# Performance work log

Measured on AMD Instinct MI355X. Metric: run time of the kernel, lower is better.

Reference implementation:

```python
import jax, jax.numpy as jnp
import numpy as np
import math

GROUPS = 32
EPS = 1e-5
NUM_HEADS = 8


def group_norm(x, gamma, beta):
    # x: [B, C, T]
    B, C, T = x.shape
    xg = x.reshape(B, GROUPS, C // GROUPS, T)
    mean = xg.mean(axis=(2, 3), keepdims=True)
    var = xg.var(axis=(2, 3), keepdims=True)
    xn = (xg - mean) * jax.lax.rsqrt(var + EPS)
    return xn.reshape(B, C, T) * gamma[None, :, None] + beta[None, :, None]


def qkv_attention(qkv, num_heads):
    # qkv: [B, 3C, T]
    B, C3, T = qkv.shape
    split = C3 // (3 * num_heads)  # head dim
    q, k, v = jnp.split(qkv, 3, axis=1)
    scale = 1.0 / math.sqrt(math.sqrt(split))
    q = (q * scale).reshape(B * num_heads, split, T)
    k = (k * scale).reshape(B * num_heads, split, T)
    v = v.reshape(B * num_heads, split, T)
    w = jnp.einsum('bct,bcs->bts', q, k)
    w = jax.nn.softmax(w.astype(jnp.float32), axis=-1).astype(w.dtype)
    out = jnp.einsum('bts,bcs->bct', w, v)
    return out.reshape(B, -1, T)


def setup_inputs() -> dict:
    key = jax.random.key(0)
    ks = jax.random.split(key, 6)
    B, C, H, W = 16, 512, 32, 32
    x = jax.random.normal(ks[0], (B, C, H, W), dtype=jnp.float32)
    gamma = jnp.ones((C,), jnp.float32)
    beta = jnp.zeros((C,), jnp.float32)
    w_qkv = jax.random.normal(ks[1], (3 * C, C), jnp.float32) * (1.0 / math.sqrt(C))
    b_qkv = jax.random.normal(ks[2], (3 * C,), jnp.float32) * 0.01
    # proj is zero-initialized in the module; use small random weights so the
    # full op chain (proj + residual) is numerically exercised.
    w_proj = jax.random.normal(ks[3], (C, C), jnp.float32) * (1.0 / math.sqrt(C))
    b_proj = jax.random.normal(ks[4], (C,), jnp.float32) * 0.01
    return {"x": x, "gamma": gamma, "beta": beta, "w_qkv": w_qkv,
            "b_qkv": b_qkv, "w_proj": w_proj, "b_proj": b_proj}


def reference(x, gamma, beta, w_qkv, b_qkv, w_proj, b_proj):
    b, c = x.shape[0], x.shape[1]
    spatial = x.shape[2:]
    xf = x.reshape(b, c, -1)                     # [B, C, T]
    xn = group_norm(xf, gamma, beta)
    qkv = jnp.einsum('oc,bct->bot', w_qkv, xn) + b_qkv[None, :, None]
    h = qkv_attention(qkv, NUM_HEADS)
    h = jnp.einsum('oc,bct->bot', w_proj, h) + b_proj[None, :, None]
    # NOTE: residual uses the normalized x (x is reassigned before norm in torch code)
    return (xn + h).reshape(b, c, *spatial)
```

## Files before the change

kernel.cpp:

```cpp
#include <hip/hip_runtime.h>

typedef __attribute__((ext_vector_type(8))) short s16x8;
typedef __attribute__((ext_vector_type(8))) unsigned short u16x8;
typedef __attribute__((ext_vector_type(4))) float f32x4;
typedef __attribute__((ext_vector_type(16))) float f32x16;

#define DEV static __device__ __forceinline__

DEV unsigned short f2bf(float f){
  union { float f; unsigned u; } v; v.f = f;
  unsigned u = v.u;
  return (unsigned short)((u + 0x7FFFu + ((u >> 16) & 1u)) >> 16);
}

DEV unsigned cvt_pk(float lo, float hi){
  unsigned r;
  asm("v_cvt_pk_bf16_f32 %0, %1, %2" : "=v"(r) : "v"(lo), "v"(hi));
  return r;
}

DEV void gload16(const void* g, void* l){
  __builtin_amdgcn_global_load_lds((const __attribute__((address_space(1))) void*)g,
                                   (__attribute__((address_space(3))) void*)l, 16, 0, 0);
}

DEV unsigned usel(bool c, unsigned a, unsigned b){ return c ? a : b; }

__global__ __launch_bounds__(256) void k_cvt(const float* __restrict__ src,
                                             unsigned short* __restrict__ dst, int n4){
  int i = blockIdx.x * 256 + threadIdx.x;
  if (i >= n4) return;
  float4 v = ((const float4*)src)[i];
  unsigned long long p = (unsigned long long)f2bf(v.x)
                       | ((unsigned long long)f2bf(v.y) << 16)
                       | ((unsigned long long)f2bf(v.z) << 32)
                       | ((unsigned long long)f2bf(v.w) << 48);
  *(unsigned long long*)(dst + (size_t)i * 4) = p;
}

__global__ __launch_bounds__(256) void k_gn(const float* __restrict__ x,
    const float* __restrict__ gamma, const float* __restrict__ beta,
    float* __restrict__ stats, unsigned short* __restrict__ xt){
  __shared__ unsigned short lt[1024 * 16];
  __shared__ float red[8];
  __shared__ float sh_ms[2];
  const int b = blockIdx.x >> 5, g = blockIdx.x & 31;
  const int tid = threadIdx.x;
  const float* base = x + ((size_t)(b * 512 + g * 16)) * 1024;

  float s = 0.f, ss = 0.f;
  #pragma unroll
  for (int i = 0; i < 16; ++i){
    float4 v = *(const float4*)(base + i * 1024 + tid * 4);
    s  += v.x + v.y + v.z + v.w;
    ss += v.x * v.x + v.y * v.y + v.z * v.z + v.w * v.w;
  }
  #pragma unroll
  for (int d = 1; d < 64; d <<= 1){ s += __shfl_xor(s, d); ss += __shfl_xor(ss, d); }
  if ((tid & 63) == 0){ red[tid >> 6] = s; red[4 + (tid >> 6)] = ss; }
  __syncthreads();
  if (tid == 0){
    float ts  = red[0] + red[1] + red[2] + red[3];
    float tss = red[4] + red[5] + red[6] + red[7];
    float mean = ts * (1.f / 16384.f);
    float var  = tss * (1.f / 16384.f) - mean * mean;
    float rstd = rsqrtf(var + 1e-5f);
    sh_ms[0] = mean; sh_ms[1] = rstd;
    stats[(size_t)blockIdx.x * 2] = mean;
    stats[(size_t)blockIdx.x * 2 + 1] = rstd;
  }
  __syncthreads();
  const float mean = sh_ms[0], rstd = sh_ms[1];

  unsigned short vals[4][16];
  #pragma unroll
  for (int i = 0; i < 16; ++i){
    float4 v = *(const float4*)(base + i * 1024 + tid * 4);
    float gsc = gamma[g * 16 + i] * rstd;
    float bof = beta[g * 16 + i] - mean * gsc;
    vals[0][i] = f2bf(v.x * gsc + bof);
    vals[1][i] = f2bf(v.y * gsc + bof);
    vals[2][i] = f2bf(v.z * gsc + bof);
    vals[3][i] = f2bf(v.w * gsc + bof);
  }
  #pragma unroll
  for (int k2 = 0; k2 < 4; ++k2){
    u16x8 lo, hi;
    #pragma unroll
    for (int e = 0; e < 8; ++e){ lo[e] = vals[k2][e]; hi[e] = vals[k2][8 + e]; }
    int t = tid * 4 + k2;
    *(u16x8*)&lt[t * 16]     = lo;
    *(u16x8*)&lt[t * 16 + 8] = hi;
  }
  __syncthreads();
  unsigned short* dst = xt + ((size_t)b * 1024) * 512 + g * 16;
  #pragma unroll
  for (int j = 0; j < 8; ++j){
    int idx = j * 256 + tid;
    int t = idx >> 1, half = idx & 1;
    u16x8 v = *(const u16x8*)&lt[t * 16 + half * 8];
    *(u16x8*)(dst + (size_t)t * 512 + half * 8) = v;
  }
}

DEV void gemm_mainloop(const unsigned short* __restrict__ pA,
                       const unsigned short* __restrict__ pB,
                       unsigned short* As, unsigned short* Bs,
                       f32x4 (&acc)[4][4], int tid){
  const int lane = tid & 63, wv = tid >> 6;
  const int wr = wv >> 1, wc = wv & 1;
  const int ro = lane & 15;
  for (int k0 = 0; k0 < 512; k0 += 64){
    #pragma unroll
    for (int it = 0; it < 4; ++it){
      int chunk = it * 256 + tid;
      int r = chunk >> 3, sb = chunk & 7;
      size_t goff = (size_t)r * 512 + k0 + ((sb ^ (r & 7)) << 3);
      gload16(pA + goff, As + (size_t)(it * 256 + wv * 64) * 8);
      gload16(pB + goff, Bs + (size_t)(it * 256 + wv * 64) * 8);
    }
    __syncthreads();
    #pragma unroll
    for (int kk = 0; kk < 2; ++kk){
      s16x8 a[4], bb[4];
      int ko = kk * 64 + ((lane >> 4) << 4);
      #pragma unroll
      for (int i2 = 0; i2 < 4; ++i2){
        int ra = wr * 64 + i2 * 16 + ro;
        a[i2]  = *(const s16x8*)((const char*)As + ra * 128 + (ko ^ ((ra & 7) << 4)));
        int rb = wc * 64 + i2 * 16 + ro;
        bb[i2] = *(const s16x8*)((const char*)Bs + rb * 128 + (ko ^ ((rb & 7) << 4)));
      }
      __builtin_amdgcn_s_setprio(1);
      #pragma unroll
      for (int i2 = 0; i2 < 4; ++i2)
        #pragma unroll
        for (int j2 = 0; j2 < 4; ++j2)
          acc[i2][j2] = __builtin_amdgcn_mfma_f32_16x16x32_bf16(a[i2], bb[j2], acc[i2][j2], 0, 0, 0);
      __builtin_amdgcn_s_setprio(0);
    }
    __syncthreads();
  }
}

__global__ __launch_bounds__(256) void k_qkv(const unsigned short* __restrict__ W,
    const unsigned short* __restrict__ Xt, const float* __restrict__ bias,
    unsigned short* __restrict__ qkt, unsigned short* __restrict__ vbuf){
  __shared__ unsigned short As[128 * 64], Bs[128 * 64];
  const int bid = blockIdx.x;
  const int nt = bid & 7; const int tmp = bid >> 3;
  const int mt = tmp % 12, b = tmp / 12;
  const int tid = threadIdx.x;
  const unsigned short* Wt = W + (size_t)mt * 128 * 512;
  const unsigned short* Xb = Xt + ((size_t)(b * 1024) + nt * 128) * 512;
  f32x4 acc[4][4];
  #pragma unroll
  for (int i = 0; i < 4; ++i)
    #pragma unroll
    for (int j = 0; j < 4; ++j) acc[i][j] = f32x4{0.f, 0.f, 0.f, 0.f};
  const bool isv = (mt >= 8);
  if (isv) gemm_mainloop(Wt, Xb, As, Bs, acc, tid);
  else     gemm_mainloop(Xb, Wt, As, Bs, acc, tid);
  const int lane = tid & 63, wv = tid >> 6, wr = wv >> 1, wc = wv & 1;
  const int col = lane & 15, rq = (lane >> 4) << 2;
  if (isv){
    #pragma unroll
    for (int i = 0; i < 4; ++i){
      #pragma unroll
      for (int jj = 0; jj < 4; ++jj){
        int og = mt * 128 + wr * 64 + i * 16 + rq + jj;
        float bv = bias[og];
        unsigned short* drow = vbuf + ((size_t)(b * 512) + (og - 1024)) * 1024 + nt * 128 + wc * 64;
        #pragma unroll
        for (int j = 0; j < 4; ++j)
          drow[j * 16 + col] = f2bf(acc[i][j][jj] + bv);
      }
    }
  } else {
    #pragma unroll
    for (int i = 0; i < 4; ++i){
      #pragma unroll
      for (int jj = 0; jj < 4; ++jj){
        int tg = nt * 128 + wr * 64 + i * 16 + rq + jj;
        unsigned short* drow = qkt + ((size_t)(b * 1024) + tg) * 1024 + mt * 128 + wc * 64;
        #pragma unroll
        for (int j = 0; j < 4; ++j){
          int og = mt * 128 + wc * 64 + j * 16 + col;
          drow[j * 16 + col] = f2bf(acc[i][j][jj] + bias[og]);
        }
      }
    }
  }
}

__global__ __launch_bounds__(256, 4) void k_attn(const unsigned short* __restrict__ qkt,
    const unsigned short* __restrict__ vbuf, unsigned short* __restrict__ ht){
  __shared__ __align__(16) unsigned short smem[8192];
  unsigned short* Ks = smem;
  unsigned short* Vs = smem + 4096;

  const int bid = blockIdx.x;
  const int xcd = bid & 7, slot = bid >> 3;
  const int qt = slot & 7;
  const int b = slot >> 3, h = xcd;
  const int tid = threadIdx.x, lane = tid & 63, wv = tid >> 6;
  const int l31 = lane & 31, hi = lane >> 5;
  const int wq0 = qt * 128 + wv * 32;
  const float CSC = 0.125f * 1.44269504f;

  s16x8 qf[4];
  {
    const unsigned short* qrow = qkt + ((size_t)(b * 1024) + wq0 + l31) * 1024 + h * 64 + hi * 8;
    #pragma unroll
    for (int kk = 0; kk < 4; ++kk)
      qf[kk] = *(const s16x8*)(qrow + kk * 16);
  }

  f32x16 o_acc[2];
  #pragma unroll
  for (int mi = 0; mi < 2; ++mi)
    #pragma unroll
    for (int e = 0; e < 16; ++e) o_acc[mi][e] = 0.f;
  float m_run = -1e30f, l_run = 0.f;

  const unsigned short* Kg = qkt + (size_t)(b * 1024) * 1024 + 512 + h * 64;
  const unsigned short* Vg = vbuf + ((size_t)(b * 512) + h * 64) * 1024;

  for (int s0 = 0; s0 < 1024; s0 += 64){
    #pragma unroll
    for (int it = 0; it < 2; ++it){
      int chunk = it * 256 + tid;
      int r = chunk >> 3, sb = chunk & 7;
      int so = (sb ^ (r & 7)) << 3;
      gload16(Kg + (size_t)(s0 + r) * 1024 + so, Ks + (size_t)(it * 256 + wv * 64) * 8);
      gload16(Vg + (size_t)r * 1024 + s0 + so,   Vs + (size_t)(it * 256 + wv * 64) * 8);
    }
    __syncthreads();

    f32x16 sa[2];
    #pragma unroll
    for (int ni = 0; ni < 2; ++ni)
      #pragma unroll
      for (int e = 0; e < 16; ++e) sa[ni][e] = 0.f;
    #pragma unroll
    for (int kk = 0; kk < 4; ++kk){
      s16x8 kf[2];
      #pragma unroll
      for (int ni = 0; ni < 2; ++ni){
        int r = ni * 32 + l31;
        kf[ni] = *(const s16x8*)((const char*)Ks + r * 128 + ((kk * 32 + hi * 16) ^ ((r & 7) << 4)));
      }
      __builtin_amdgcn_s_setprio(1);
      sa[0] = __builtin_amdgcn_mfma_f32_32x32x16_bf16(kf[0], qf[kk], sa[0], 0, 0, 0);
      sa[1] = __builtin_amdgcn_mfma_f32_32x32x16_bf16(kf[1], qf[kk], sa[1], 0, 0, 0);
      __builtin_amdgcn_s_setprio(0);
    }

    float mx = -1e30f;
    #pragma unroll
    for (int ni = 0; ni < 2; ++ni)
      #pragma unroll
      for (int e = 0; e < 16; ++e) mx = fmaxf(mx, sa[ni][e]);
    mx = fmaxf(mx, __shfl_xor(mx, 32));
    float mxs = mx * CSC;
    if (__any(mxs > m_run + 8.f)){
      float mnew = fmaxf(m_run, mxs);
      float alpha = exp2f(m_run - mnew);
      m_run = mnew;
      l_run *= alpha;
      #pragma unroll
      for (int mi = 0; mi < 2; ++mi)
        #pragma unroll
        for (int e = 0; e < 16; ++e) o_acc[mi][e] *= alpha;
    }
    float rs = 0.f;
    unsigned pk[2][4][2];
    #pragma unroll
    for (int ni = 0; ni < 2; ++ni)
      #pragma unroll
      for (int rr = 0; rr < 4; ++rr){
        float p0 = exp2f(fmaf(sa[ni][4 * rr + 0], CSC, -m_run));
        float p1 = exp2f(fmaf(sa[ni][4 * rr + 1], CSC, -m_run));
        float p2 = exp2f(fmaf(sa[ni][4 * rr + 2], CSC, -m_run));
        float p3 = exp2f(fmaf(sa[ni][4 * rr + 3], CSC, -m_run));
        rs += (p0 + p1) + (p2 + p3);
        pk[ni][rr][0] = cvt_pk(p0, p1);
        pk[ni][rr][1] = cvt_pk(p2, p3);
      }
    rs += __shfl_xor(rs, 32);
    l_run += rs;

    #pragma unroll
    for (int ks = 0; ks < 4; ++ks){
      int ni = ks >> 1, q2 = (ks & 1) * 2;
      unsigned L0 = pk[ni][q2][0],     L1 = pk[ni][q2][1];
      unsigned H0 = pk[ni][q2 + 1][0], H1 = pk[ni][q2 + 1][1];
      unsigned rL0 = __shfl_xor((int)L0, 32), rL1 = __shfl_xor((int)L1, 32);
      unsigned rH0 = __shfl_xor((int)H0, 32), rH1 = __shfl_xor((int)H1, 32);
      union { unsigned u[4]; s16x8 v; } pb;
      pb.u[0] = usel(hi, rH0, L0);
      pb.u[1] = usel(hi, rH1, L1);
      pb.u[2] = usel(hi, H0, rL0);
      pb.u[3] = usel(hi, H1, rL1);
      s16x8 vf[2];
      #pragma unroll
      for (int mi = 0; mi < 2; ++mi){
        int c = mi * 32 + l31;
        vf[mi] = *(const s16x8*)((const char*)Vs + c * 128 + ((ks * 32 + hi * 16) ^ ((c & 7) << 4)));
      }
      __builtin_amdgcn_s_setprio(1);
      o_acc[0] = __builtin_amdgcn_mfma_f32_32x32x16_bf16(vf[0], pb.v, o_acc[0], 0, 0, 0);
      o_acc[1] = __builtin_amdgcn_mfma_f32_32x32x16_bf16(vf[1], pb.v, o_acc[1], 0, 0, 0);
      __builtin_amdgcn_s_setprio(0);
    }
    __syncthreads();
  }

  float invl = 1.f / l_run;
  unsigned short* ow = smem + wv * 2048;
  int t = l31;
  #pragma unroll
  for (int mi = 0; mi < 2; ++mi)
    #pragma unroll
    for (int rr = 0; rr < 4; ++rr){
      int c0 = mi * 32 + 8 * rr + 4 * hi;
      unsigned d0 = cvt_pk(o_acc[mi][4 * rr + 0] * invl, o_acc[mi][4 * rr + 1] * invl);
      unsigned d1 = cvt_pk(o_acc[mi][4 * rr + 2] * invl, o_acc[mi][4 * rr + 3] * invl);
      unsigned* dst = (unsigned*)(ow + t * 64 + (c0 ^ ((t & 7) << 3)));
      dst[0] = d0; dst[1] = d1;
    }
  __syncthreads();
  unsigned short* hbase = ht + ((size_t)(b * 1024) + wq0) * 512 + h * 64;
  #pragma unroll
  for (int i = 0; i < 4; ++i){
    int id = i * 64 + lane;
    int tl = id >> 3, c8 = id & 7;
    u16x8 v = *(const u16x8*)(ow + tl * 64 + ((c8 ^ (tl & 7)) << 3));
    *(u16x8*)(hbase + (size_t)tl * 512 + c8 * 8) = v;
  }
}

__global__ __launch_bounds__(256) void k_proj(const unsigned short* __restrict__ Wp,
    const unsigned short* __restrict__ Ht, const float* __restrict__ bias,
    const float* __restrict__ x, const float* __restrict__ stats,
    const float* __restrict__ gamma, const float* __restrict__ beta,
    float* __restrict__ out){
  __shared__ unsigned short As[128 * 64], Bs[128 * 64];
  const int bid = blockIdx.x;
  const int nt = bid & 7, mt = (bid >> 3) & 3, b = bid >> 5;
  const int tid = threadIdx.x;
  f32x4 acc[4][4];
  #pragma unroll
  for (int i = 0; i < 4; ++i)
    #pragma unroll
    for (int j = 0; j < 4; ++j) acc[i][j] = f32x4{0.f, 0.f, 0.f, 0.f};
  gemm_mainloop(Wp + (size_t)mt * 128 * 512,
                Ht + ((size_t)(b * 1024) + nt * 128) * 512, As, Bs, acc, tid);
  const int lane = tid & 63, wv = tid >> 6, wr = wv >> 1, wc = wv & 1;
  const int col = lane & 15, rq = (lane >> 4) << 2;
  #pragma unroll
  for (int i = 0; i < 4; ++i){
    #pragma unroll
    for (int jj = 0; jj < 4; ++jj){
      int og = mt * 128 + wr * 64 + i * 16 + rq + jj;
      float mean = stats[(size_t)(b * 32 + (og >> 4)) * 2];
      float rstd = stats[(size_t)(b * 32 + (og >> 4)) * 2 + 1];
      float gsc = gamma[og] * rstd;
      float bof = beta[og] - mean * gsc + bias[og];
      const float* xrow = x  + ((size_t)(b * 512) + og) * 1024 + nt * 128 + wc * 64;
      float* orow      = out + ((size_t)(b * 512) + og) * 1024 + nt * 128 + wc * 64;
      #pragma unroll
      for (int j = 0; j < 4; ++j){
        float xv = xrow[j * 16 + col];
        orow[j * 16 + col] = acc[i][j][jj] + xv * gsc + bof;
      }
    }
  }
}

extern "C" void kernel_launch(void* const* d_in, const int* in_sizes, int n_in,
                              void* d_out, int out_size, void* d_ws, size_t ws_size,
                              hipStream_t stream) {
  (void)in_sizes; (void)n_in; (void)out_size; (void)ws_size;
  const float* x      = (const float*)d_in[0];
  const float* gamma  = (const float*)d_in[1];
  const float* beta   = (const float*)d_in[2];
  const float* w_qkv  = (const float*)d_in[3];
  const float* b_qkv  = (const float*)d_in[4];
  const float* w_proj = (const float*)d_in[5];
  const float* b_proj = (const float*)d_in[6];
  float* out = (float*)d_out;
  char* ws = (char*)d_ws;

  unsigned short* wq_bf = (unsigned short*)ws;
  unsigned short* wp_bf = (unsigned short*)(ws + 1572864);
  float*          stats = (float*)(ws + 2097152);
  unsigned short* Xt    = (unsigned short*)(ws + 2101248);
  unsigned short* qkt   = (unsigned short*)(ws + 18878464);
  unsigned short* vbuf  = (unsigned short*)(ws + 52432896);

  k_cvt<<<768, 256, 0, stream>>>(w_qkv, wq_bf, 196608);
  k_cvt<<<256, 256, 0, stream>>>(w_proj, wp_bf, 65536);
  k_gn<<<512, 256, 0, stream>>>(x, gamma, beta, stats, Xt);
  k_qkv<<<1536, 256, 0, stream>>>(wq_bf, Xt, b_qkv, qkt, vbuf);
  unsigned short* Ht = Xt;
  k_attn<<<1024, 256, 0, stream>>>(qkt, vbuf, Ht);
  k_proj<<<512, 256, 0, stream>>>(wp_bf, Ht, b_proj, x, stats, gamma, beta, out);
}
```

Measured before the change: 141.4 us.

## Double-buffer K/V tiles in attention and reuse loaded x in group norm

The attention kernel now keeps two LDS buffers for K/V tiles and issues the async global-to-LDS loads for the next tile before computing the current one, waiting on vmcnt only at the end of each iteration. This is meant to hide global-load latency behind the MFMA work. The group-norm kernel keeps the 16 loaded float4 values in registers instead of reading x from global memory a second time. The cost is twice the LDS per attention block, which may lower occupancy, and more registers in the group-norm kernel.

After: 142.0 us. No clear change (+0.4%).

```diff
diff --git a/kernel.cpp b/kernel.cpp
--- a/kernel.cpp
+++ b/kernel.cpp
@@ -48,12 +48,13 @@
   const int tid = threadIdx.x;
   const float* base = x + ((size_t)(b * 512 + g * 16)) * 1024;
 
+  float4 vv[16];
   float s = 0.f, ss = 0.f;
   #pragma unroll
   for (int i = 0; i < 16; ++i){
-    float4 v = *(const float4*)(base + i * 1024 + tid * 4);
-    s  += v.x + v.y + v.z + v.w;
-    ss += v.x * v.x + v.y * v.y + v.z * v.z + v.w * v.w;
+    vv[i] = *(const float4*)(base + i * 1024 + tid * 4);
+    s  += vv[i].x + vv[i].y + vv[i].z + vv[i].w;
+    ss += vv[i].x * vv[i].x + vv[i].y * vv[i].y + vv[i].z * vv[i].z + vv[i].w * vv[i].w;
   }
   #pragma unroll
   for (int d = 1; d < 64; d <<= 1){ s += __shfl_xor(s, d); ss += __shfl_xor(ss, d); }
@@ -75,13 +76,12 @@
   unsigned short vals[4][16];
   #pragma unroll
   for (int i = 0; i < 16; ++i){
-    float4 v = *(const float4*)(base + i * 1024 + tid * 4);
     float gsc = gamma[g * 16 + i] * rstd;
     float bof = beta[g * 16 + i] - mean * gsc;
-    vals[0][i] = f2bf(v.x * gsc + bof);
-    vals[1][i] = f2bf(v.y * gsc + bof);
-    vals[2][i] = f2bf(v.z * gsc + bof);
-    vals[3][i] = f2bf(v.w * gsc + bof);
+    vals[0][i] = f2bf(vv[i].x * gsc + bof);
+    vals[1][i] = f2bf(vv[i].y * gsc + bof);
+    vals[2][i] = f2bf(vv[i].z * gsc + bof);
+    vals[3][i] = f2bf(vv[i].w * gsc + bof);
   }
   #pragma unroll
   for (int k2 = 0; k2 < 4; ++k2){
@@ -195,9 +195,7 @@
 
 __global__ __launch_bounds__(256, 4) void k_attn(const unsigned short* __restrict__ qkt,
     const unsigned short* __restrict__ vbuf, unsigned short* __restrict__ ht){
-  __shared__ __align__(16) unsigned short smem[8192];
-  unsigned short* Ks = smem;
-  unsigned short* Vs = smem + 4096;
+  __shared__ __align__(16) unsigned short smem[16384];
 
   const int bid = blockIdx.x;
   const int xcd = bid & 7, slot = bid >> 3;
@@ -226,16 +224,27 @@
   const unsigned short* Kg = qkt + (size_t)(b * 1024) * 1024 + 512 + h * 64;
   const unsigned short* Vg = vbuf + ((size_t)(b * 512) + h * 64) * 1024;
 
-  for (int s0 = 0; s0 < 1024; s0 += 64){
-    #pragma unroll
-    for (int it = 0; it < 2; ++it){
-      int chunk = it * 256 + tid;
-      int r = chunk >> 3, sb = chunk & 7;
-      int so = (sb ^ (r & 7)) << 3;
-      gload16(Kg + (size_t)(s0 + r) * 1024 + so, Ks + (size_t)(it * 256 + wv * 64) * 8);
-      gload16(Vg + (size_t)r * 1024 + s0 + so,   Vs + (size_t)(it * 256 + wv * 64) * 8);
-    }
-    __syncthreads();
+  #define STAGE(s0, bsel) do {                                                          \
+    unsigned short* Kd = smem + (bsel) * 8192;                                          \
+    unsigned short* Vd = Kd + 4096;                                                     \
+    _Pragma("unroll")                                                                   \
+    for (int it = 0; it < 2; ++it){                                                     \
+      int chunk = it * 256 + tid;                                                       \
+      int r = chunk >> 3, sb = chunk & 7;                                               \
+      int so = (sb ^ (r & 7)) << 3;                                                     \
+      gload16(Kg + (size_t)((s0) + r) * 1024 + so, Kd + (size_t)(it * 256 + wv * 64) * 8); \
+      gload16(Vg + (size_t)r * 1024 + (s0) + so,   Vd + (size_t)(it * 256 + wv * 64) * 8); \
+    }                                                                                   \
+  } while (0)
+
+  STAGE(0, 0);
+  __syncthreads();
+  int cur = 0;
+
+  for (int t = 0; t < 16; ++t){
+    if (t < 15) STAGE((t + 1) * 64, cur ^ 1);
+    const unsigned short* Ks = smem + cur * 8192;
+    const unsigned short* Vs = Ks + 4096;
 
     f32x16 sa[2];
     #pragma unroll
@@ -313,8 +322,13 @@
       o_acc[1] = __builtin_amdgcn_mfma_f32_32x32x16_bf16(vf[1], pb.v, o_acc[1], 0, 0, 0);
       __builtin_amdgcn_s_setprio(0);
     }
+
+    asm volatile("s_waitcnt vmcnt(0)" ::: "memory");
+    __builtin_amdgcn_sched_barrier(0);
     __syncthreads();
-  }
+    cur ^= 1;
+  }
+  #undef STAGE
 
   float invl = 1.f / l_run;
   unsigned short* ow = smem + wv * 2048;
```
